# Performance work log

Hardware: AMD Instinct MI355X
Metric: run time of the kernel (lower is better)

Reference implementation:

```python
import jax, jax.numpy as jnp
import numpy as np

D_MODEL = 1024
D_K = 64
D_V = 64
N_HEADS = 16
B, S = 2, 2048


def setup_inputs() -> dict:
    key = jax.random.key(0)
    ks = jax.random.split(key, 12)
    scale = 1.0 / np.sqrt(D_MODEL)
    inp = {
        "Q": jax.random.normal(ks[0], (B, S, D_MODEL), jnp.float32),
        "K": jax.random.normal(ks[1], (B, S, D_MODEL), jnp.float32),
        "V": jax.random.normal(ks[2], (B, S, D_MODEL), jnp.float32),
        # per-head projection weights (stacked over heads) and biases
        "Wq": jax.random.normal(ks[3], (N_HEADS, D_MODEL, D_K), jnp.float32) * scale,
        "bq": jax.random.normal(ks[4], (N_HEADS, D_K), jnp.float32) * 0.01,
        "Wk": jax.random.normal(ks[5], (N_HEADS, D_MODEL, D_K), jnp.float32) * scale,
        "bk": jax.random.normal(ks[6], (N_HEADS, D_K), jnp.float32) * 0.01,
        "Wv": jax.random.normal(ks[7], (N_HEADS, D_MODEL, D_V), jnp.float32) * scale,
        "bv": jax.random.normal(ks[8], (N_HEADS, D_V), jnp.float32) * 0.01,
        # output projection: (n_heads*d_v) -> d_model
        "Wo": jax.random.normal(ks[9], (N_HEADS * D_V, D_MODEL), jnp.float32) / np.sqrt(N_HEADS * D_V),
        "bo": jax.random.normal(ks[10], (D_MODEL,), jnp.float32) * 0.01,
    }
    return inp


def reference(Q, K, V, Wq, bq, Wk, bk, Wv, bv, Wo, bo):
    # Per-head projections, vectorized over heads: [B,H,S,dk]
    QW = jnp.einsum("bsd,hdk->bhsk", Q, Wq) + bq[None, :, None, :]
    KW = jnp.einsum("bsd,hdk->bhsk", K, Wk) + bk[None, :, None, :]
    VW = jnp.einsum("bsd,hdv->bhsv", V, Wv) + bv[None, :, None, :]
    # scores: [B,H,S,S]
    scores = jnp.einsum("bhsk,bhtk->bhst", QW, KW)
    # Faithful to torch source: softmax FIRST, then divide by d_k, then by 2
    attn = jax.nn.softmax(scores, axis=-1) / D_K / 2.0
    ctx = jnp.einsum("bhst,bhtv->bhsv", attn, VW)  # [B,H,S,dv]
    # concat heads along last dim (head order == torch concat order)
    ctx = jnp.transpose(ctx, (0, 2, 1, 3)).reshape(B, S, N_HEADS * D_V)
    return ctx @ Wo + bo
```

## Files before the change

### kernel.cpp

```cpp
#include <hip/hip_runtime.h>

typedef unsigned short u16;
typedef unsigned int u32;
typedef __attribute__((ext_vector_type(8))) short bf16x8;
typedef __attribute__((ext_vector_type(4))) float f32x4;

__device__ __forceinline__ u16 f2b(float f) {
    union { float f; u32 u; } v; v.f = f;
    return (u16)((v.u + 0x7FFF + ((v.u >> 16) & 1)) >> 16);
}

__device__ __forceinline__ void glds16(const u16* g, u16* l) {
    __builtin_amdgcn_global_load_lds(
        (const __attribute__((address_space(1))) void*)g,
        (__attribute__((address_space(3))) void*)l, 16, 0, 0);
}

__global__ __launch_bounds__(256) void prep(
    const float* __restrict__ Q, const float* __restrict__ K,
    const float* __restrict__ V,
    const float* __restrict__ Wq, const float* __restrict__ Wk,
    const float* __restrict__ Wv, const float* __restrict__ Wo,
    u16* __restrict__ Qb, u16* __restrict__ Kb, u16* __restrict__ Vb,
    u16* __restrict__ WqT, u16* __restrict__ WkT, u16* __restrict__ WvT,
    u16* __restrict__ WoT)
{
    __shared__ float t[64][68];
    const int z = blockIdx.z, x = blockIdx.x, tid = threadIdx.x;

    if (z < 3) {
        const float* in = (z == 0) ? Q : (z == 1) ? K : V;
        u16* out = (z == 0) ? Qb : (z == 1) ? Kb : Vb;
        const int n4 = 1048576;
        const int stride = 1024 * 256;
        for (int i = x * 256 + tid; i < n4; i += stride) {
            float4 v = ((const float4*)in)[i];
            ushort4 o;
            o.x = f2b(v.x); o.y = f2b(v.y); o.z = f2b(v.z); o.w = f2b(v.w);
            ((ushort4*)out)[i] = o;
        }
        return;
    }

    const int rr = tid >> 4, c4 = (tid & 15) * 4;

    if (z == 3) {
        if (x >= 768) return;
        const int sel = x >> 8, hz = (x >> 4) & 15;
        const float* in = (sel == 0) ? Wq : (sel == 1) ? Wk : Wv;
        u16* out = (sel == 0) ? WqT : (sel == 1) ? WkT : WvT;
        const long mb = (long)hz * 65536;
        const int r0 = (x & 15) * 64;

        #pragma unroll
        for (int p = 0; p < 4; ++p) {
            float4 v = *(const float4*)(in + mb + (long)(r0 + p * 16 + rr) * 64 + c4);
            *(float4*)&t[p * 16 + rr][c4] = v;
        }
        __syncthreads();
        #pragma unroll
        for (int p = 0; p < 4; ++p) {
            const int oc = p * 16 + rr;
            const int r4 = (tid & 15) * 4;
            ushort4 o;
            o.x = f2b(t[r4 + 0][oc]); o.y = f2b(t[r4 + 1][oc]);
            o.z = f2b(t[r4 + 2][oc]); o.w = f2b(t[r4 + 3][oc]);
            *(ushort4*)(out + mb + (long)oc * 1024 + r0 + r4) = o;
        }
        return;
    }

    if (x >= 256) return;
    const int r0 = (x & 15) * 64, c0 = (x >> 4) * 64;
    #pragma unroll
    for (int p = 0; p < 4; ++p) {
        float4 v = *(const float4*)(Wo + (long)(r0 + p * 16 + rr) * 1024 + c0 + c4);
        *(float4*)&t[p * 16 + rr][c4] = v;
    }
    __syncthreads();
    #pragma unroll
    for (int p = 0; p < 4; ++p) {
        const int oc = p * 16 + rr;
        const int r4 = (tid & 15) * 4;
        ushort4 o;
        o.x = f2b(t[r4 + 0][oc]); o.y = f2b(t[r4 + 1][oc]);
        o.z = f2b(t[r4 + 2][oc]); o.w = f2b(t[r4 + 3][oc]);
        *(ushort4*)(WoT + (long)(c0 + oc) * 1024 + r0 + r4) = o;
    }
}

#define GEMM_STAGE(A_, BT_, p_, k_)                                            \
    _Pragma("unroll")                                                          \
    for (int i2 = 0; i2 < 4; ++i2) {                                           \
        const int i = w * 4 + i2;                                              \
        glds16(A_ + ga + (long)i * 8 * 1024 + (k_), &As[p_][i * 512]);         \
        glds16(BT_ + gb + (long)i * 8 * 1024 + (k_), &Bs[p_][i * 512]);        \
    }

#define GEMM_CORE(A_, BT_)                                                     \
    __shared__ u16 As[2][128 * 64];                                            \
    __shared__ u16 Bs[2][128 * 64];                                            \
    const int tid = threadIdx.x, lane = tid & 63, w = tid >> 6;                \
    const int m0 = blockIdx.x * 128, n0 = blockIdx.y * 128;                    \
    const int wm = (w >> 1) * 64, wn = (w & 1) * 64;                           \
    const int fr = lane & 15, quad = lane >> 4;                                \
    f32x4 acc[4][4];                                                           \
    const f32x4 zero = {0.f, 0.f, 0.f, 0.f};                                   \
    _Pragma("unroll")                                                          \
    for (int mi = 0; mi < 4; ++mi)                                             \
        _Pragma("unroll")                                                      \
        for (int ni = 0; ni < 4; ++ni) acc[mi][ni] = zero;                     \
    const int srow = lane >> 3;                                                \
    const int schk = (lane & 7) ^ (srow & 7);       \
    const long ga = (long)(m0 + srow) * 1024 + schk * 8;                       \
    const long gb = (long)(n0 + srow) * 1024 + schk * 8;                       \
    const int f7 = fr & 7;                                                     \
    GEMM_STAGE(A_, BT_, 0, 0)                                                  \
    __syncthreads();                                                           \
    for (int k0 = 0; k0 < 1024; k0 += 64) {                                    \
        const int p = (k0 >> 6) & 1;                                           \
        if (k0 + 64 < 1024) { GEMM_STAGE(A_, BT_, p ^ 1, k0 + 64) }            \
        __builtin_amdgcn_s_setprio(1);                                         \
        _Pragma("unroll")                                                      \
        for (int kc = 0; kc < 2; ++kc) {                                       \
            const int pos = ((kc * 4 + quad) ^ f7) * 8;                        \
            bf16x8 af[4], bfr[4];                                              \
            _Pragma("unroll")                                                  \
            for (int mi = 0; mi < 4; ++mi)                                     \
                af[mi] = *(const bf16x8*)&As[p][(wm + mi * 16 + fr) * 64 + pos]; \
            _Pragma("unroll")                                                  \
            for (int ni = 0; ni < 4; ++ni)                                     \
                bfr[ni] = *(const bf16x8*)&Bs[p][(wn + ni * 16 + fr) * 64 + pos]; \
            _Pragma("unroll")                                                  \
            for (int mi = 0; mi < 4; ++mi)                                     \
                _Pragma("unroll")                                              \
                for (int ni = 0; ni < 4; ++ni)                                 \
                    acc[mi][ni] = __builtin_amdgcn_mfma_f32_16x16x32_bf16(     \
                        af[mi], bfr[ni], acc[mi][ni], 0, 0, 0);                \
        }                                                                      \
        __builtin_amdgcn_s_setprio(0);                                         \
        __syncthreads();                                                       \
    }

__global__ __launch_bounds__(256) void proj3(
    const u16* __restrict__ Qb, const u16* __restrict__ Kb,
    const u16* __restrict__ Vb,
    const u16* __restrict__ WqT, const u16* __restrict__ WkT,
    const u16* __restrict__ WvT,
    const float* __restrict__ bq, const float* __restrict__ bk,
    const float* __restrict__ bv,
    u16* __restrict__ QWb, u16* __restrict__ KWb, u16* __restrict__ VWb)
{
    const int z = blockIdx.z;
    const u16* A  = (z == 0) ? Qb : (z == 1) ? Kb : Vb;
    const u16* BT = (z == 0) ? WqT : (z == 1) ? WkT : WvT;
    const float* bias = (z == 0) ? bq : (z == 1) ? bk : bv;
    u16* Cu = (z == 0) ? QWb : (z == 1) ? KWb : VWb;
    const float scl = (z == 0) ? 1.4426950408889634f : 1.0f;

    GEMM_CORE(A, BT)

    #pragma unroll
    for (int mi = 0; mi < 4; ++mi) {
        #pragma unroll
        for (int ni = 0; ni < 4; ++ni) {
            const int mB = m0 + wm + mi * 16 + quad * 4;
            const int c  = n0 + wn + ni * 16 + fr;
            const int b = mB >> 11, s = mB & 2047, h = c >> 6, k = c & 63;
            const float bi = bias[c];
            if (z != 2) {
                #pragma unroll
                for (int r = 0; r < 4; ++r)
                    Cu[((long)(b * 16 + h) * 2048 + s + r) * 64 + k] =
                        f2b((acc[mi][ni][r] + bi) * scl);
            } else {
                ushort4 o;
                o.x = f2b(acc[mi][ni][0] + bi);
                o.y = f2b(acc[mi][ni][1] + bi);
                o.z = f2b(acc[mi][ni][2] + bi);
                o.w = f2b(acc[mi][ni][3] + bi);
                *(ushort4*)&Cu[((long)(b * 16 + h) * 64 + k) * 2048 + s] = o;
            }
        }
    }
}

__global__ __launch_bounds__(256) void gemm_out(
    const u16* __restrict__ A, const u16* __restrict__ BT,
    const float* __restrict__ bias, float* __restrict__ Cf)
{
    GEMM_CORE(A, BT)

    #pragma unroll
    for (int mi = 0; mi < 4; ++mi) {
        #pragma unroll
        for (int ni = 0; ni < 4; ++ni) {
            #pragma unroll
            for (int r = 0; r < 4; ++r) {
                const int m = m0 + wm + mi * 16 + quad * 4 + r;
                const int c = n0 + wn + ni * 16 + fr;
                Cf[(long)m * 1024 + c] = acc[mi][ni][r] + bias[c];
            }
        }
    }
}

__global__ __launch_bounds__(256) void attn_mfma(
    const u16* __restrict__ QW, const u16* __restrict__ KW,
    const u16* __restrict__ VW, u16* __restrict__ ctxb)
{
    __shared__ u16 kt[3][64 * 64];
    __shared__ u16 vt[3][64 * 64];
    __shared__ u16 ps[4][32 * 72];

    const int tid = threadIdx.x, lane = tid & 63, w = tid >> 6;
    const int id = blockIdx.x + gridDim.x * blockIdx.y;
    const int bh = (id & 7) * 4 + ((id >> 3) & 3);
    const int q0 = (id >> 5) * 128;
    const int b = bh >> 4, h = bh & 15;
    const int fr = lane & 15, quad = lane >> 4;
    const int f7 = fr & 7;

    bf16x8 aQ[2][2];
    #pragma unroll
    for (int s = 0; s < 2; ++s) {
        const u16* qp = QW + ((long)bh * 2048 + q0 + w * 32 + s * 16 + fr) * 64;
        aQ[s][0] = *(const bf16x8*)(qp + quad * 8);
        aQ[s][1] = *(const bf16x8*)(qp + 32 + quad * 8);
    }

    const f32x4 zero = {0.f, 0.f, 0.f, 0.f};
    f32x4 acc[2][4], lac[2];
    #pragma unroll
    for (int s = 0; s < 2; ++s) {
        lac[s] = zero;
        #pragma unroll
        for (int d = 0; d < 4; ++d) acc[s][d] = zero;
    }
    bf16x8 bones;
    #pragma unroll
    for (int j = 0; j < 8; ++j) bones[j] = (short)0x3F80;

    const int srow = lane >> 3;
    const int schk = (lane & 7) ^ (srow & 7);
    const long kgb = (long)bh * (2048 * 64);
    const long vgb = (long)bh * (64 * 2048);

#define ATTN_STAGE(p_, t_)                                                    \
    _Pragma("unroll")                                                         \
    for (int i2 = 0; i2 < 2; ++i2) {                                          \
        const int i = w * 2 + i2;                                             \
        glds16(KW + kgb + (long)((t_) + i * 8 + srow) * 64 + schk * 8,        \
               &kt[p_][i * 512]);                                             \
        glds16(VW + vgb + (long)(i * 8 + srow) * 2048 + (t_) + schk * 8,      \
               &vt[p_][i * 512]);                                             \
    }

    ATTN_STAGE(0, 0)
    ATTN_STAGE(1, 64)

    const int pos0 = (quad ^ f7) * 8;
    const int pos1 = pos0 ^ 32;
    u16* pw = ps[w];

    for (int t0 = 0; t0 < 2048; t0 += 64) {
        const int it = t0 >> 6;
        const int p = it % 3;

        if (t0 + 64 < 2048) {
            __asm__ volatile("s_waitcnt vmcnt(4)" ::: "memory");
        } else {
            __asm__ volatile("s_waitcnt vmcnt(0)" ::: "memory");
        }
        __builtin_amdgcn_s_barrier();
        __asm__ volatile("" ::: "memory");
        __builtin_amdgcn_sched_barrier(0);

        if (t0 + 128 < 2048) { ATTN_STAGE((it + 2) % 3, t0 + 128) }

        const u16* ktp = kt[p];
        const u16* vtp = vt[p];

        f32x4 sc[2][4];
        __builtin_amdgcn_s_setprio(1);
        #pragma unroll
        for (int s = 0; s < 2; ++s) {
            #pragma unroll
            for (int sub = 0; sub < 4; ++sub) {
                const int row = (sub * 16 + fr) * 64;
                bf16x8 k0 = *(const bf16x8*)&ktp[row + pos0];
                bf16x8 k1 = *(const bf16x8*)&ktp[row + pos1];
                f32x4 z = __builtin_amdgcn_mfma_f32_16x16x32_bf16(k0, aQ[s][0], zero, 0, 0, 0);
                sc[s][sub] = __builtin_amdgcn_mfma_f32_16x16x32_bf16(k1, aQ[s][1], z, 0, 0, 0);
            }
        }
        __builtin_amdgcn_s_setprio(0);

        #pragma unroll
        for (int s = 0; s < 2; ++s) {
            #pragma unroll
            for (int sub = 0; sub < 4; ++sub) {
                float e0 = __builtin_amdgcn_exp2f(sc[s][sub][0]);
                float e1 = __builtin_amdgcn_exp2f(sc[s][sub][1]);
                float e2 = __builtin_amdgcn_exp2f(sc[s][sub][2]);
                float e3 = __builtin_amdgcn_exp2f(sc[s][sub][3]);
                u32 lo, hi;
                asm("v_cvt_pk_bf16_f32 %0, %1, %2" : "=v"(lo) : "v"(e0), "v"(e1));
                asm("v_cvt_pk_bf16_f32 %0, %1, %2" : "=v"(hi) : "v"(e2), "v"(e3));
                uint2 pk2; pk2.x = lo; pk2.y = hi;
                *(uint2*)&pw[(s * 16 + fr) * 72 + sub * 16 + quad * 4] = pk2;
            }
        }
        __asm__ volatile("s_waitcnt lgkmcnt(0)" ::: "memory");

        __builtin_amdgcn_s_setprio(1);
        #pragma unroll
        for (int s = 0; s < 2; ++s) {
            const bf16x8 aP0 = *(const bf16x8*)&pw[(s * 16 + fr) * 72 + quad * 8];
            const bf16x8 aP1 = *(const bf16x8*)&pw[(s * 16 + fr) * 72 + 32 + quad * 8];
            lac[s] = __builtin_amdgcn_mfma_f32_16x16x32_bf16(aP0, bones, lac[s], 0, 0, 0);
            lac[s] = __builtin_amdgcn_mfma_f32_16x16x32_bf16(aP1, bones, lac[s], 0, 0, 0);
            #pragma unroll
            for (int d = 0; d < 4; ++d) {
                const int row = (d * 16 + fr) * 64;
                bf16x8 v0 = *(const bf16x8*)&vtp[row + pos0];
                bf16x8 v1 = *(const bf16x8*)&vtp[row + pos1];
                acc[s][d] = __builtin_amdgcn_mfma_f32_16x16x32_bf16(aP0, v0, acc[s][d], 0, 0, 0);
                acc[s][d] = __builtin_amdgcn_mfma_f32_16x16x32_bf16(aP1, v1, acc[s][d], 0, 0, 0);
            }
        }
        __builtin_amdgcn_s_setprio(0);
    }

    #pragma unroll
    for (int s = 0; s < 2; ++s) {
        #pragma unroll
        for (int r = 0; r < 4; ++r) {
            const float scl = 1.0f / (lac[s][r] * 128.0f);
            const long row = (long)b * 2048 + q0 + w * 32 + s * 16 + quad * 4 + r;
            #pragma unroll
            for (int d = 0; d < 4; ++d)
                ctxb[row * 1024 + h * 64 + d * 16 + fr] = f2b(acc[s][d][r] * scl);
        }
    }
}

extern "C" void kernel_launch(void* const* d_in, const int* in_sizes, int n_in,
                              void* d_out, int out_size, void* d_ws, size_t ws_size,
                              hipStream_t stream) {
    (void)in_sizes; (void)n_in; (void)out_size; (void)ws_size;

    const float* Q  = (const float*)d_in[0];
    const float* K  = (const float*)d_in[1];
    const float* V  = (const float*)d_in[2];
    const float* Wq = (const float*)d_in[3];
    const float* bq = (const float*)d_in[4];
    const float* Wk = (const float*)d_in[5];
    const float* bk = (const float*)d_in[6];
    const float* Wv = (const float*)d_in[7];
    const float* bv = (const float*)d_in[8];
    const float* Wo = (const float*)d_in[9];
    const float* bo = (const float*)d_in[10];
    float* out = (float*)d_out;

    u16* ws  = (u16*)d_ws;
    u16* Qb  = ws;
    u16* Kb  = Qb  + 4194304;
    u16* Vb  = Kb  + 4194304;
    u16* WqT = Vb  + 4194304;
    u16* WkT = WqT + 1048576;
    u16* WvT = WkT + 1048576;
    u16* WoT = WvT + 1048576;
    u16* QWb = WoT + 1048576;
    u16* KWb = QWb + 4194304;
    u16* VWb = KWb + 4194304;
    u16* ctx = VWb + 4194304;

    prep<<<dim3(1024, 1, 5), 256, 0, stream>>>(Q, K, V, Wq, Wk, Wv, Wo,
                                               Qb, Kb, Vb, WqT, WkT, WvT, WoT);

    proj3<<<dim3(32, 8, 3), 256, 0, stream>>>(Qb, Kb, Vb, WqT, WkT, WvT,
                                              bq, bk, bv, QWb, KWb, VWb);

    attn_mfma<<<dim3(16, 32), 256, 0, stream>>>(QWb, KWb, VWb, ctx);

    gemm_out<<<dim3(32, 8), 256, 0, stream>>>(ctx, WoT, bo, out);
}
```

Measured before the change: 218.9 us.

## Single-buffer GEMM LDS staging and shrink output GEMM tile to 128x64

Replaces double-buffered LDS prefetch in the projection GEMMs with a single buffer loaded between two barriers, halving shared memory per block to allow more resident blocks. The output projection GEMM gets a dedicated 128x64 tile kernel with twice as many blocks to better fill the CUs. This gives up overlap of global loads with MFMA compute within a block, relying on occupancy to hide latency instead.

```diff
diff --git a/kernel.cpp b/kernel.cpp
--- a/kernel.cpp
+++ b/kernel.cpp
@@ -89,17 +89,17 @@
     }
 }
 
-#define GEMM_STAGE(A_, BT_, p_, k_)                                            \
+#define GEMM_STAGE_SB(A_, BT_, k_)                                             \
     _Pragma("unroll")                                                          \
     for (int i2 = 0; i2 < 4; ++i2) {                                           \
         const int i = w * 4 + i2;                                              \
-        glds16(A_ + ga + (long)i * 8 * 1024 + (k_), &As[p_][i * 512]);         \
-        glds16(BT_ + gb + (long)i * 8 * 1024 + (k_), &Bs[p_][i * 512]);        \
-    }
-
-#define GEMM_CORE(A_, BT_)                                                     \
-    __shared__ u16 As[2][128 * 64];                                            \
-    __shared__ u16 Bs[2][128 * 64];                                            \
+        glds16(A_ + ga + (long)i * 8 * 1024 + (k_), &As[i * 512]);             \
+        glds16(BT_ + gb + (long)i * 8 * 1024 + (k_), &Bs[i * 512]);            \
+    }
+
+#define GEMM_CORE_SB(A_, BT_)                                                  \
+    __shared__ u16 As[128 * 64];                                               \
+    __shared__ u16 Bs[128 * 64];                                               \
     const int tid = threadIdx.x, lane = tid & 63, w = tid >> 6;                \
     const int m0 = blockIdx.x * 128, n0 = blockIdx.y * 128;                    \
     const int wm = (w >> 1) * 64, wn = (w & 1) * 64;                           \
@@ -115,11 +115,10 @@
     const long ga = (long)(m0 + srow) * 1024 + schk * 8;                       \
     const long gb = (long)(n0 + srow) * 1024 + schk * 8;                       \
     const int f7 = fr & 7;                                                     \
-    GEMM_STAGE(A_, BT_, 0, 0)                                                  \
-    __syncthreads();                                                           \
     for (int k0 = 0; k0 < 1024; k0 += 64) {                                    \
-        const int p = (k0 >> 6) & 1;                                           \
-        if (k0 + 64 < 1024) { GEMM_STAGE(A_, BT_, p ^ 1, k0 + 64) }            \
+        __syncthreads();                                                       \
+        GEMM_STAGE_SB(A_, BT_, k0)                                             \
+        __syncthreads();                                                       \
         __builtin_amdgcn_s_setprio(1);                                         \
         _Pragma("unroll")                                                      \
         for (int kc = 0; kc < 2; ++kc) {                                       \
@@ -127,10 +126,10 @@
             bf16x8 af[4], bfr[4];                                              \
             _Pragma("unroll")                                                  \
             for (int mi = 0; mi < 4; ++mi)                                     \
-                af[mi] = *(const bf16x8*)&As[p][(wm + mi * 16 + fr) * 64 + pos]; \
+                af[mi] = *(const bf16x8*)&As[(wm + mi * 16 + fr) * 64 + pos];  \
             _Pragma("unroll")                                                  \
             for (int ni = 0; ni < 4; ++ni)                                     \
-                bfr[ni] = *(const bf16x8*)&Bs[p][(wn + ni * 16 + fr) * 64 + pos]; \
+                bfr[ni] = *(const bf16x8*)&Bs[(wn + ni * 16 + fr) * 64 + pos]; \
             _Pragma("unroll")                                                  \
             for (int mi = 0; mi < 4; ++mi)                                     \
                 _Pragma("unroll")                                              \
@@ -139,7 +138,6 @@
                         af[mi], bfr[ni], acc[mi][ni], 0, 0, 0);                \
         }                                                                      \
         __builtin_amdgcn_s_setprio(0);                                         \
-        __syncthreads();                                                       \
     }
 
 __global__ __launch_bounds__(256) void proj3(
@@ -158,7 +156,7 @@
     u16* Cu = (z == 0) ? QWb : (z == 1) ? KWb : VWb;
     const float scl = (z == 0) ? 1.4426950408889634f : 1.0f;
 
-    GEMM_CORE(A, BT)
+    GEMM_CORE_SB(A, BT)
 
     #pragma unroll
     for (int mi = 0; mi < 4; ++mi) {
@@ -189,12 +187,64 @@
     const u16* __restrict__ A, const u16* __restrict__ BT,
     const float* __restrict__ bias, float* __restrict__ Cf)
 {
-    GEMM_CORE(A, BT)
+    __shared__ u16 As[128 * 64];
+    __shared__ u16 Bs[64 * 64];
+
+    const int tid = threadIdx.x, lane = tid & 63, w = tid >> 6;
+    const int m0 = blockIdx.x * 128, n0 = blockIdx.y * 64;
+    const int wm = (w >> 1) * 64, wn = (w & 1) * 32;
+    const int fr = lane & 15, quad = lane >> 4;
+    f32x4 acc[4][2];
+    const f32x4 zero = {0.f, 0.f, 0.f, 0.f};
+    #pragma unroll
+    for (int mi = 0; mi < 4; ++mi)
+        #pragma unroll
+        for (int ni = 0; ni < 2; ++ni) acc[mi][ni] = zero;
+
+    const int srow = lane >> 3;
+    const int schk = (lane & 7) ^ (srow & 7);
+    const long ga = (long)(m0 + srow) * 1024 + schk * 8;
+    const long gb = (long)(n0 + srow) * 1024 + schk * 8;
+    const int f7 = fr & 7;
+
+    for (int k0 = 0; k0 < 1024; k0 += 64) {
+        __syncthreads();
+        #pragma unroll
+        for (int i2 = 0; i2 < 4; ++i2) {
+            const int i = w * 4 + i2;
+            glds16(A + ga + (long)i * 8 * 1024 + k0, &As[i * 512]);
+        }
+        #pragma unroll
+        for (int i2 = 0; i2 < 2; ++i2) {
+            const int i = w * 2 + i2;
+            glds16(BT + gb + (long)i * 8 * 1024 + k0, &Bs[i * 512]);
+        }
+        __syncthreads();
+        __builtin_amdgcn_s_setprio(1);
+        #pragma unroll
+        for (int kc = 0; kc < 2; ++kc) {
+            const int pos = ((kc * 4 + quad) ^ f7) * 8;
+            bf16x8 af[4], bfr[2];
+            #pragma unroll
+            for (int mi = 0; mi < 4; ++mi)
+                af[mi] = *(const bf16x8*)&As[(wm + mi * 16 + fr) * 64 + pos];
+            #pragma unroll
+            for (int ni = 0; ni < 2; ++ni)
+                bfr[ni] = *(const bf16x8*)&Bs[(wn + ni * 16 + fr) * 64 + pos];
+            #pragma unroll
+            for (int mi = 0; mi < 4; ++mi)
+                #pragma unroll
+                for (int ni = 0; ni < 2; ++ni)
+                    acc[mi][ni] = __builtin_amdgcn_mfma_f32_16x16x32_bf16(
+                        af[mi], bfr[ni], acc[mi][ni], 0, 0, 0);
+        }
+        __builtin_amdgcn_s_setprio(0);
+    }
 
     #pragma unroll
     for (int mi = 0; mi < 4; ++mi) {
         #pragma unroll
-        for (int ni = 0; ni < 4; ++ni) {
+        for (int ni = 0; ni < 2; ++ni) {
             #pragma unroll
             for (int r = 0; r < 4; ++r) {
                 const int m = m0 + wm + mi * 16 + quad * 4 + r;
@@ -384,5 +434,5 @@
 
     attn_mfma<<<dim3(16, 32), 256, 0, stream>>>(QWb, KWb, VWb, ctx);
 
-    gemm_out<<<dim3(32, 8), 256, 0, stream>>>(ctx, WoT, bo, out);
-}
+    gemm_out<<<dim3(32, 16), 256, 0, stream>>>(ctx, WoT, bo, out);
+}
```

Measured after the change: 218.7 us. Within noise of the previous version (-0.1%).
